# Performance work log

Measured on AMD Instinct MI355X. Metric: run time of the kernel, lower is better.

## Reference

```python
import jax, jax.numpy as jnp
import numpy as np

D_MODEL, D_INNER, D_STATE, HEADDIM, NHEADS, D_CONV, EPS = 2048, 4096, 64, 64, 64, 4, 1e-5
CONV_DIM = D_INNER + 2 * D_STATE  # ngroups=1


def setup_inputs() -> dict:
    key = jax.random.key(0)
    ks = jax.random.split(key, 8)
    return {
        "hidden_states": jax.random.normal(ks[0], (2, 2048, D_MODEL), jnp.float32),
        "rms_weight": jnp.ones((D_MODEL,), jnp.float32),
        "in_proj_w": jax.random.normal(ks[1], (2 * D_INNER + 2 * D_STATE + NHEADS, D_MODEL), jnp.float32) * 0.02,
        "conv_w": jax.random.normal(ks[2], (CONV_DIM, D_CONV), jnp.float32) * 0.2,
        "conv_b": jnp.zeros((CONV_DIM,), jnp.float32),
        "dt_bias": jax.random.normal(ks[3], (NHEADS,), jnp.float32) * 0.5,
        "A_log": jax.random.uniform(ks[4], (NHEADS,), jnp.float32, 0.0, 1.0),
        "D": jnp.ones((NHEADS,), jnp.float32),
        "norm_w": jnp.ones((D_INNER,), jnp.float32),
        "out_proj_w": jax.random.normal(ks[5], (D_MODEL, D_INNER), jnp.float32) * 0.02,
    }


def _rmsnorm(x, w, eps=EPS):
    var = jnp.mean(jnp.square(x), axis=-1, keepdims=True)
    return x * jax.lax.rsqrt(var + eps) * w


def reference(hidden_states, rms_weight, in_proj_w, conv_w, conv_b, dt_bias, A_log, D, norm_w, out_proj_w):
    b, l, _ = hidden_states.shape
    residual = hidden_states
    u = _rmsnorm(hidden_states, rms_weight)
    zxbcdt = jnp.einsum("bld,ed->ble", u, in_proj_w)
    z = zxbcdt[..., :D_INNER]
    xBC = zxbcdt[..., D_INNER:D_INNER + CONV_DIM]
    dt = zxbcdt[..., D_INNER + CONV_DIM:]  # (b, l, h)

    # causal depthwise conv1d over seq
    xBC_t = jnp.transpose(xBC, (0, 2, 1))  # (b, c, l)
    kernel = conv_w[:, None, :]  # (c, 1, k)
    xBC_t = jax.lax.conv_general_dilated(
        xBC_t, kernel, window_strides=(1,), padding=[(D_CONV - 1, 0)],
        feature_group_count=CONV_DIM,
        dimension_numbers=("NCH", "OIH", "NCH"))
    xBC = jax.nn.silu(jnp.transpose(xBC_t, (0, 2, 1)) + conv_b)

    x = xBC[..., :D_INNER].reshape(b, l, NHEADS, HEADDIM)
    B = xBC[..., D_INNER:D_INNER + D_STATE]  # (b, l, n)
    C = xBC[..., D_INNER + D_STATE:]         # (b, l, n)

    dt = jax.nn.softplus(dt + dt_bias)  # (b, l, h)
    A = -jnp.exp(A_log)                 # (h,)
    dA = jnp.exp(dt * A)                # (b, l, h)

    # sequential selective scan over time
    def step(state, inp):
        dA_t, dt_t, x_t, B_t, C_t = inp  # (b,h), (b,h), (b,h,p), (b,n), (b,n)
        state = state * dA_t[:, :, None, None] + jnp.einsum(
            "bh,bhp,bn->bhpn", dt_t, x_t, B_t)
        y_t = jnp.einsum("bhpn,bn->bhp", state, C_t)
        return state, y_t

    xs = (jnp.moveaxis(dA, 1, 0), jnp.moveaxis(dt, 1, 0),
          jnp.moveaxis(x, 1, 0), jnp.moveaxis(B, 1, 0), jnp.moveaxis(C, 1, 0))
    state0 = jnp.zeros((b, NHEADS, HEADDIM, D_STATE), hidden_states.dtype)
    _, ys = jax.lax.scan(step, state0, xs)
    y = jnp.moveaxis(ys, 0, 1)  # (b, l, h, p)
    y = y + D[None, None, :, None] * x
    y = y.reshape(b, l, D_INNER)

    # gated RMSNorm, then output projection
    y = _rmsnorm(y * jax.nn.silu(z), norm_w)
    out = jnp.einsum("ble,de->bld", y, out_proj_w)
    return residual + out
```

## Files before the change

### kernel.cpp

```cpp
#include <hip/hip_runtime.h>
#include <stdint.h>

#define DEV static __device__ __forceinline__

typedef __attribute__((ext_vector_type(8))) __bf16 bf16x8;
typedef __attribute__((ext_vector_type(4))) float f32x4;
typedef __attribute__((ext_vector_type(16))) float f32x16;

DEV float b2f(unsigned short u) {
    union { unsigned int i; float f; } v; v.i = ((unsigned int)u) << 16; return v.f;
}
DEV unsigned short f2b(float f) {
    unsigned int u = __builtin_bit_cast(unsigned int, f);
    unsigned int r = (u + 0x7FFFu + ((u >> 16) & 1u)) >> 16;
    return (unsigned short)r;
}
DEV f32x4 mfma16(bf16x8 a, bf16x8 b, f32x4 c) {
    return __builtin_amdgcn_mfma_f32_16x16x32_bf16(a, b, c, 0, 0, 0);
}
DEV f32x16 mfma32(bf16x8 a, bf16x8 b, f32x16 c) {
    return __builtin_amdgcn_mfma_f32_32x32x16_bf16(a, b, c, 0, 0, 0);
}

DEV void gload16(const void* g, void* l) {
    __builtin_amdgcn_global_load_lds(
        (const __attribute__((address_space(1))) void*)g,
        (__attribute__((address_space(3))) void*)l, 16, 0, 0);
}

__global__ __launch_bounds__(256) void k_cvt(
    const float* __restrict__ src, unsigned short* __restrict__ dst)
{
    long i = ((long)blockIdx.x * 256 + threadIdx.x) * 8;
    float4 a = *(const float4*)(src + i);
    float4 b = *(const float4*)(src + i + 4);
    union { uint4 v; unsigned short s[8]; } o;
    o.s[0] = f2b(a.x); o.s[1] = f2b(a.y); o.s[2] = f2b(a.z); o.s[3] = f2b(a.w);
    o.s[4] = f2b(b.x); o.s[5] = f2b(b.y); o.s[6] = f2b(b.z); o.s[7] = f2b(b.w);
    *(uint4*)(dst + i) = o.v;
}

__global__ __launch_bounds__(256) void k_rmsnorm_in(
    const float* __restrict__ h, const float* __restrict__ w,
    unsigned short* __restrict__ u)
{
    int row = blockIdx.x, t = threadIdx.x;
    const float* hp = h + (long)row * 2048 + t * 8;
    float4 a = *(const float4*)hp;
    float4 b = *(const float4*)(hp + 4);
    float x[8] = {a.x, a.y, a.z, a.w, b.x, b.y, b.z, b.w};
    float ss = 0.f;
#pragma unroll
    for (int i = 0; i < 8; i++) ss += x[i] * x[i];
#pragma unroll
    for (int o = 32; o > 0; o >>= 1) ss += __shfl_down(ss, o);
    __shared__ float red[4];
    if ((t & 63) == 0) red[t >> 6] = ss;
    __syncthreads();
    float tot = red[0] + red[1] + red[2] + red[3];
    float scale = rsqrtf(tot * (1.0f / 2048.0f) + 1e-5f);
    float4 wa = *(const float4*)(w + t * 8);
    float4 wb = *(const float4*)(w + t * 8 + 4);
    float wv[8] = {wa.x, wa.y, wa.z, wa.w, wb.x, wb.y, wb.z, wb.w};
    union { uint4 v; unsigned short s[8]; } ow;
#pragma unroll
    for (int i = 0; i < 8; i++) ow.s[i] = f2b(x[i] * scale * wv[i]);
    *(uint4*)(u + (long)row * 2048 + t * 8) = ow.v;
}

__global__ __launch_bounds__(512, 2) void k_gemm256(
    const unsigned short* __restrict__ A, const unsigned short* __restrict__ Bm,
    int K, unsigned short* __restrict__ Cb, int ldc)
{
    __shared__ __align__(16) char lds[131072];
    int tid = threadIdx.x;
    int w = tid >> 6, l = tid & 63;
    int NT = K >> 6, NI = K >> 7;
    long Kb = (long)K * 2;

    int nwg = gridDim.x * gridDim.y;
    int cpx = nwg >> 3;
    int fl = blockIdx.y * gridDim.x + blockIdx.x;
    int swz = (fl & 7) * cpx + (fl >> 3);
    long m0 = (long)(swz % gridDim.x) * 256;
    long n0 = (long)(swz / gridDim.x) * 256;

    int rl = tid >> 3;
    int csw16 = (((tid & 7) ^ (rl & 7)) << 4);
    const char* pA0 = (const char*)A + (m0 + rl) * Kb + csw16;
    const char* pA1 = (const char*)A + (m0 + 64 + rl) * Kb + csw16;
    const char* pB0 = (const char*)Bm + (n0 + rl) * Kb + csw16;
    const char* pB1 = (const char*)Bm + (n0 + 64 + rl) * Kb + csw16;
    int ldst = tid * 16;

#define STG(P0, P1, RGN, kt, half) do { if ((kt) < NT) {                      \
    char* Lr_ = lds + (((kt) & 1) << 16) + (RGN) + ((half) << 14);            \
    long go_ = (long)(half) * 128 * Kb + (long)(kt) * 128;                    \
    gload16((P0) + go_, Lr_ + ldst);                                          \
    gload16((P1) + go_, Lr_ + 8192 + ldst); } } while (0)

    int lq = l >> 4, lr15 = l & 15, key = l & 7;
    int off0 = ((lq ^ key) << 4);
    int off1 = (((4 + lq) ^ key) << 4);
    int aB = ((w >> 2) * 128 + lr15) * 128;
    int bB = 32768 + (((w & 3) * 64 + lr15) * 128);

    bf16x8 aF[4][2], b0F[2][2], b1F[2][2];
    f32x4 acc[8][4];
#pragma unroll
    for (int s = 0; s < 8; s++)
#pragma unroll
        for (int t = 0; t < 4; t++) acc[s][t] = (f32x4){0.f, 0.f, 0.f, 0.f};

#define DS_A(mh, BUF) do {                                                    \
    const char* ba_ = lds + (BUF) + aB + (mh) * 8192;                         \
    _Pragma("unroll") for (int s_ = 0; s_ < 4; s_++) {                        \
        aF[s_][0] = *(const bf16x8*)(ba_ + s_ * 2048 + off0);                 \
        aF[s_][1] = *(const bf16x8*)(ba_ + s_ * 2048 + off1); } } while (0)

#define DS_B(DST, nh, BUF) do {                                               \
    const char* bb_ = lds + (BUF) + bB + (nh) * 4096;                         \
    _Pragma("unroll") for (int t_ = 0; t_ < 2; t_++) {                        \
        DST[t_][0] = *(const bf16x8*)(bb_ + t_ * 2048 + off0);                \
        DST[t_][1] = *(const bf16x8*)(bb_ + t_ * 2048 + off1); } } while (0)

#define MQ(mh, nh, BF) do {                                                   \
    __builtin_amdgcn_s_setprio(1);                                            \
    _Pragma("unroll") for (int kk_ = 0; kk_ < 2; kk_++)                       \
    _Pragma("unroll") for (int s_ = 0; s_ < 4; s_++)                          \
    _Pragma("unroll") for (int t_ = 0; t_ < 2; t_++)                          \
        acc[(mh) * 4 + s_][(nh) * 2 + t_] =                                   \
            mfma16(aF[s_][kk_], BF[t_][kk_], acc[(mh) * 4 + s_][(nh) * 2 + t_]); \
    __builtin_amdgcn_s_setprio(0); } while (0)

#define BAR asm volatile("s_barrier" ::: "memory")
#define LGD asm volatile("s_waitcnt lgkmcnt(0)" ::: "memory")

    STG(pA0, pA1, 0,     0, 0);
    STG(pA0, pA1, 0,     0, 1);
    STG(pB0, pB1, 32768, 0, 0);
    STG(pB0, pB1, 32768, 0, 1);
    STG(pB0, pB1, 32768, 1, 0);
    STG(pB0, pB1, 32768, 1, 1);
    STG(pA0, pA1, 0,     1, 0);
    asm volatile("s_waitcnt vmcnt(6)" ::: "memory");
    BAR;

    for (int it = 0; it < NI; ++it) {
        int k1 = 2 * it + 1, k2 = 2 * it + 2, k3 = 2 * it + 3;
        DS_A(0, 0); DS_B(b0F, 0, 0);
        STG(pA0, pA1, 0, k1, 1);
        BAR; MQ(0, 0, b0F); LGD; BAR;
        DS_B(b1F, 1, 0);
        BAR; MQ(0, 1, b1F); LGD; BAR;
        DS_A(1, 0);
        STG(pB0, pB1, 32768, k2, 0);
        BAR; MQ(1, 1, b1F); LGD; BAR;
        STG(pB0, pB1, 32768, k2, 1);
        BAR; MQ(1, 0, b0F);
        if (it == NI - 1) { asm volatile("s_waitcnt vmcnt(0)" ::: "memory"); }
        else              { asm volatile("s_waitcnt vmcnt(4)" ::: "memory"); }
        BAR;
        DS_A(0, 65536); DS_B(b0F, 0, 65536);
        STG(pA0, pA1, 0, k2, 0);
        BAR; MQ(0, 0, b0F); LGD; BAR;
        DS_B(b1F, 1, 65536);
        STG(pA0, pA1, 0, k2, 1);
        BAR; MQ(0, 1, b1F); LGD; BAR;
        DS_A(1, 65536);
        STG(pB0, pB1, 32768, k3, 0);
        BAR; MQ(1, 1, b1F); LGD; BAR;
        STG(pB0, pB1, 32768, k3, 1);
        STG(pA0, pA1, 0, k3, 0);
        BAR; MQ(1, 0, b0F);
        if (it < NI - 1) { asm volatile("s_waitcnt vmcnt(6)" ::: "memory"); }
        BAR;
    }

    int colb = (w & 3) * 64 + lr15;
    int rowb = (w >> 2) * 128 + lq * 4;
#pragma unroll
    for (int s = 0; s < 8; s++)
#pragma unroll
        for (int t = 0; t < 4; t++) {
            long col = n0 + colb + t * 16;
            long row = m0 + rowb + s * 16;
#pragma unroll
            for (int r = 0; r < 4; r++)
                Cb[(row + r) * ldc + col] = f2b(acc[s][t][r]);
        }
#undef STG
#undef DS_A
#undef DS_B
#undef MQ
#undef BAR
#undef LGD
}

template <int EPI>
__global__ __launch_bounds__(256) void k_gemm_bt(
    const unsigned short* __restrict__ A, const unsigned short* __restrict__ Bm,
    int K, int nvalid, unsigned short* __restrict__ Cb, float* __restrict__ Cf,
    int ldc, const float* __restrict__ Res)
{
    __shared__ __align__(16) unsigned short sA[128 * 64];
    __shared__ __align__(16) unsigned short sB[128 * 64];
    int t = threadIdx.x;
    int w = t >> 6, L = t & 63;

    int flat = blockIdx.y * gridDim.x + blockIdx.x;
    int per = gridDim.x * 8;
    int strip = flat / per;
    int rem = flat - strip * per;
    long m0 = (long)(strip * 8 + (rem & 7)) * 128;
    long n0 = (long)(rem >> 3) * 128;

    int rloc = t >> 3;
    int c16  = t & 7;
    int csw  = c16 ^ (rloc & 7);
    const unsigned short* gAp[4];
    const unsigned short* gBp[4];
#pragma unroll
    for (int i = 0; i < 4; i++) {
        gAp[i] = A + (m0 + i * 32 + rloc) * (long)K + csw * 8;
        long rb = n0 + i * 32 + rloc;
        if (rb >= nvalid) rb = nvalid - 1;
        gBp[i] = Bm + rb * (long)K + csw * 8;
    }
    unsigned short* lA = sA + t * 8;
    unsigned short* lB = sB + t * 8;

    int mw = (w >> 1) * 64, nw = (w & 1) * 64;
    int rowA = mw + (L & 31), rowB = nw + (L & 31);
    int swA = (rowA & 7) << 4, swB = (rowB & 7) << 4;
    int q16 = (L >> 5) * 16;
    const char* pA = (const char*)sA + rowA * 128;
    const char* pB = (const char*)sB + rowB * 128;

    f32x16 acc[2][2];
#pragma unroll
    for (int ti = 0; ti < 2; ti++)
#pragma unroll
        for (int tj = 0; tj < 2; tj++)
#pragma unroll
            for (int r = 0; r < 16; r++) acc[ti][tj][r] = 0.f;

    for (int kt = 0; kt < K; kt += 64) {
#pragma unroll
        for (int i = 0; i < 4; i++) {
            gload16(gAp[i], lA + i * 2048);
            gload16(gBp[i], lB + i * 2048);
            gAp[i] += 64; gBp[i] += 64;
        }
        __syncthreads();
#pragma unroll
        for (int kk = 0; kk < 4; kk++) {
            bf16x8 af[2], bf[2];
#pragma unroll
            for (int ti = 0; ti < 2; ti++)
                af[ti] = *(const bf16x8*)(pA + ti * 4096 + ((q16 + kk * 32) ^ swA));
#pragma unroll
            for (int tj = 0; tj < 2; tj++)
                bf[tj] = *(const bf16x8*)(pB + tj * 4096 + ((q16 + kk * 32) ^ swB));
#pragma unroll
            for (int ti = 0; ti < 2; ti++)
#pragma unroll
                for (int tj = 0; tj < 2; tj++)
                    acc[ti][tj] = mfma32(af[ti], bf[tj], acc[ti][tj]);
        }
        __syncthreads();
    }
    int colL = L & 31;
    int rL = (L >> 5) * 4;
#pragma unroll
    for (int ti = 0; ti < 2; ti++)
#pragma unroll
        for (int tj = 0; tj < 2; tj++) {
            long c = n0 + nw + tj * 32 + colL;
            if (c >= nvalid) continue;
#pragma unroll
            for (int r = 0; r < 16; r++) {
                long row = m0 + mw + ti * 32 + (r & 3) + 8 * (r >> 2) + rL;
                float v = acc[ti][tj][r];
                if (EPI == 0) Cb[row * ldc + c] = f2b(v);
                else          Cf[row * ldc + c] = v + Res[row * ldc + c];
            }
        }
}

__global__ __launch_bounds__(128) void k_conv(
    const unsigned short* __restrict__ zx, const float* __restrict__ cw,
    const float* __restrict__ cb, unsigned short* __restrict__ xbc)
{
    int c = blockIdx.x * 128 + threadIdx.x;
    int b = blockIdx.z;
    int l0 = blockIdx.y * 64;
    float w0 = cw[c * 4 + 0], w1 = cw[c * 4 + 1];
    float w2 = cw[c * 4 + 2], w3 = cw[c * 4 + 3];
    float bias = cb[c];
    const unsigned short* src = zx + ((long)b * 2048) * 8384 + 4096 + c;
    float xm3 = (l0 >= 3) ? b2f(src[(long)(l0 - 3) * 8384]) : 0.f;
    float xm2 = (l0 >= 2) ? b2f(src[(long)(l0 - 2) * 8384]) : 0.f;
    float xm1 = (l0 >= 1) ? b2f(src[(long)(l0 - 1) * 8384]) : 0.f;
    const unsigned short* s2 = src + (long)l0 * 8384;
    unsigned short* dst = xbc + ((long)(b * 2048 + l0)) * 4224 + c;
#pragma unroll 8
    for (int i = 0; i < 64; i++) {
        float xl = b2f(*s2); s2 += 8384;
        float a = xm3 * w0 + xm2 * w1 + xm1 * w2 + xl * w3 + bias;
        a = a / (1.f + expf(-a));
        *dst = f2b(a); dst += 4224;
        xm3 = xm2; xm2 = xm1; xm1 = xl;
    }
}

__global__ __launch_bounds__(256) void k_chunk_state_mfma(
    const unsigned short* __restrict__ xbc, const unsigned short* __restrict__ zxdt,
    const float* __restrict__ dt_bias, const float* __restrict__ A_log,
    unsigned short* __restrict__ Sbuf, float* __restrict__ dAtot)
{
    int blk = blockIdx.x;
    int c = blk & 7, bh = blk >> 3;
    int b = bh >> 6, h = bh & 63;
    int tid = threadIdx.x;
    int w = tid >> 6, L = tid & 63;
    int quad = L >> 4, col = L & 15;
    int rowBlk = (w >> 1) * 32, colBlk = (w & 1) * 32;
    __shared__ __align__(16) unsigned short sXp[64 * 72];
    __shared__ __align__(16) unsigned short sBn[64 * 72];
    __shared__ float sdt[64], sL[64];
    float Ah = expf(A_log[h]);
    float dtb = dt_bias[h];
    f32x4 acc[2][2];
#pragma unroll
    for (int ti = 0; ti < 2; ti++)
#pragma unroll
        for (int tj = 0; tj < 2; tj++) acc[ti][tj] = (f32x4){0.f, 0.f, 0.f, 0.f};
    float sumL = 0.f;

    for (int sub = 0; sub < 4; sub++) {
        int l0 = c * 256 + sub * 64;
        {
            int t = tid >> 2, pc = tid & 3;
            const unsigned short* gX = xbc + (long)(b * 2048 + l0 + t) * 4224 + h * 64 + pc * 16;
            union { uint4 v; unsigned short s[8]; } x0, x1;
            x0.v = *(const uint4*)gX; x1.v = *(const uint4*)(gX + 8);
#pragma unroll
            for (int j = 0; j < 8; j++) {
                sXp[(pc * 16 + j) * 72 + t] = x0.s[j];
                sXp[(pc * 16 + 8 + j) * 72 + t] = x1.s[j];
            }
        }
        if (tid < 64) {
            float raw = b2f(zxdt[((long)(b * 2048 + l0 + tid)) * 8384 + 8320 + h]) + dtb;
            float dtv = (raw > 20.f) ? raw : log1pf(expf(raw));
            float cum = dtv;
#pragma unroll
            for (int off = 1; off < 64; off <<= 1) {
                float v = __shfl_up(cum, off);
                if (tid >= off) cum += v;
            }
            sdt[tid] = dtv;
            sL[tid] = -Ah * cum;
        }
        __syncthreads();
        float Lend = sL[63];
        {
            int t = tid >> 2, nc = tid & 3;
            float wt = sdt[t] * __expf(Lend - sL[t]);
            const unsigned short* gB = xbc + (long)(b * 2048 + l0 + t) * 4224 + 4096 + nc * 16;
            union { uint4 v; unsigned short s[8]; } x0, x1;
            x0.v = *(const uint4*)gB; x1.v = *(const uint4*)(gB + 8);
#pragma unroll
            for (int j = 0; j < 8; j++) {
                sBn[(nc * 16 + j) * 72 + t] = f2b(b2f(x0.s[j]) * wt);
                sBn[(nc * 16 + 8 + j) * 72 + t] = f2b(b2f(x1.s[j]) * wt);
            }
        }
        __syncthreads();
        float e_end = __expf(Lend);
        sumL += Lend;
#pragma unroll
        for (int ti = 0; ti < 2; ti++)
#pragma unroll
            for (int tj = 0; tj < 2; tj++)
#pragma unroll
                for (int r = 0; r < 4; r++) acc[ti][tj][r] *= e_end;
#pragma unroll
        for (int kb = 0; kb < 2; kb++) {
            bf16x8 ax[2], bx[2];
#pragma unroll
            for (int ti = 0; ti < 2; ti++)
                ax[ti] = *(const bf16x8*)(sXp + (rowBlk + ti * 16 + col) * 72 + kb * 32 + quad * 8);
#pragma unroll
            for (int tj = 0; tj < 2; tj++)
                bx[tj] = *(const bf16x8*)(sBn + (colBlk + tj * 16 + col) * 72 + kb * 32 + quad * 8);
#pragma unroll
            for (int ti = 0; ti < 2; ti++)
#pragma unroll
                for (int tj = 0; tj < 2; tj++)
                    acc[ti][tj] = mfma16(ax[ti], bx[tj], acc[ti][tj]);
        }
        __syncthreads();
    }
#pragma unroll
    for (int ti = 0; ti < 2; ti++)
#pragma unroll
        for (int tj = 0; tj < 2; tj++)
#pragma unroll
            for (int r = 0; r < 4; r++) {
                int p = rowBlk + ti * 16 + quad * 4 + r;
                int n = colBlk + tj * 16 + col;
                Sbuf[(long)blk * 4096 + p * 64 + n] = f2b(acc[ti][tj][r]);
            }
    if (tid == 0) dAtot[blk] = __expf(sumL);
}

__global__ __launch_bounds__(256) void k_scan_chunk_mfma(
    const unsigned short* __restrict__ xbc, const unsigned short* __restrict__ zxdt,
    const float* __restrict__ dt_bias, const float* __restrict__ A_log,
    const float* __restrict__ Dv,
    const unsigned short* __restrict__ Sbuf, const float* __restrict__ dAtot,
    unsigned short* __restrict__ yout)
{
    int blk = blockIdx.x;
    int c = blk & 7, bh = blk >> 3;
    int b = bh >> 6, h = bh & 63;
    int tid = threadIdx.x;
    int w = tid >> 6, L = tid & 63;
    int quad = L >> 4, col = L & 15;
    int rowBlk = (w >> 1) * 32, colBlk = (w & 1) * 32;
    __shared__ __align__(16) unsigned short sCm[64 * 72];
    __shared__ __align__(16) unsigned short sBtMs[64 * 72];
    __shared__ __align__(16) unsigned short sXp[64 * 72];
    __shared__ __align__(16) unsigned short sBn[64 * 72];
    __shared__ __align__(16) unsigned short sHb[64 * 72];
    __shared__ float sdt[64], sL[64], sEs[64];
    float Ah = expf(A_log[h]);
    float dtb = dt_bias[h];
    float Dh = Dv[h];

    f32x4 acc_h[2][2];
#pragma unroll
    for (int ti = 0; ti < 2; ti++)
#pragma unroll
        for (int tj = 0; tj < 2; tj++) acc_h[ti][tj] = (f32x4){0.f, 0.f, 0.f, 0.f};
    int sb = bh * 8;
    for (int j = 0; j < c; j++) {
        float d = dAtot[sb + j];
        const unsigned short* Sp = Sbuf + (long)(sb + j) * 4096;
#pragma unroll
        for (int ti = 0; ti < 2; ti++)
#pragma unroll
            for (int tj = 0; tj < 2; tj++)
#pragma unroll
                for (int r = 0; r < 4; r++) {
                    int p = rowBlk + ti * 16 + quad * 4 + r;
                    int n = colBlk + tj * 16 + col;
                    acc_h[ti][tj][r] = acc_h[ti][tj][r] * d + b2f(Sp[p * 64 + n]);
                }
    }

    for (int sub = 0; sub < 4; sub++) {
        int l0 = c * 256 + sub * 64;
        {
            int row = tid >> 2, c4 = tid & 3;
            const unsigned short* gR = xbc + (long)(b * 2048 + l0 + row) * 4224;
            uint4 v0 = *(const uint4*)(gR + 4160 + c4 * 8);
            uint4 v1 = *(const uint4*)(gR + 4160 + (c4 + 4) * 8);
            *(uint4*)(sCm + row * 72 + c4 * 8) = v0;
            *(uint4*)(sCm + row * 72 + (c4 + 4) * 8) = v1;
            uint4 w0 = *(const uint4*)(gR + 4096 + c4 * 8);
            uint4 w1 = *(const uint4*)(gR + 4096 + (c4 + 4) * 8);
            *(uint4*)(sBtMs + row * 72 + c4 * 8) = w0;
            *(uint4*)(sBtMs + row * 72 + (c4 + 4) * 8) = w1;
        }
        {
            int t = tid >> 2, pc = tid & 3;
            const unsigned short* gX = xbc + (long)(b * 2048 + l0 + t) * 4224 + h * 64 + pc * 16;
            union { uint4 v; unsigned short s[8]; } x0, x1;
            x0.v = *(const uint4*)gX; x1.v = *(const uint4*)(gX + 8);
#pragma unroll
            for (int j = 0; j < 8; j++) {
                sXp[(pc * 16 + j) * 72 + t] = x0.s[j];
                sXp[(pc * 16 + 8 + j) * 72 + t] = x1.s[j];
            }
        }
        if (tid < 64) {
            float raw = b2f(zxdt[((long)(b * 2048 + l0 + tid)) * 8384 + 8320 + h]) + dtb;
            float dtv = (raw > 20.f) ? raw : log1pf(expf(raw));
            float cum = dtv;
#pragma unroll
            for (int off = 1; off < 64; off <<= 1) {
                float v = __shfl_up(cum, off);
                if (tid >= off) cum += v;
            }
            sdt[tid] = dtv;
            float l = -Ah * cum;
            sL[tid] = l;
            sEs[tid] = __expf(l);
        }
        __syncthreads();
        float Lend = sL[63];
        {
            int t = tid >> 2, nc = tid & 3;
            float wt = sdt[t] * __expf(Lend - sL[t]);
            const unsigned short* gB = xbc + (long)(b * 2048 + l0 + t) * 4224 + 4096 + nc * 16;
            union { uint4 v; unsigned short s[8]; } x0, x1;
            x0.v = *(const uint4*)gB; x1.v = *(const uint4*)(gB + 8);
#pragma unroll
            for (int j = 0; j < 8; j++) {
                sBn[(nc * 16 + j) * 72 + t] = f2b(b2f(x0.s[j]) * wt);
                sBn[(nc * 16 + 8 + j) * 72 + t] = f2b(b2f(x1.s[j]) * wt);
            }
        }
#pragma unroll
        for (int ti = 0; ti < 2; ti++)
#pragma unroll
            for (int tj = 0; tj < 2; tj++)
#pragma unroll
                for (int r = 0; r < 4; r++) {
                    int p = rowBlk + ti * 16 + quad * 4 + r;
                    int n = colBlk + tj * 16 + col;
                    sHb[p * 72 + n] = f2b(acc_h[ti][tj][r]);
                }
        __syncthreads();
        f32x4 g[2][2];
#pragma unroll
        for (int ti = 0; ti < 2; ti++)
#pragma unroll
            for (int tj = 0; tj < 2; tj++) g[ti][tj] = (f32x4){0.f, 0.f, 0.f, 0.f};
#pragma unroll
        for (int kb = 0; kb < 2; kb++) {
            bf16x8 ac[2], bc[2];
#pragma unroll
            for (int ti = 0; ti < 2; ti++)
                ac[ti] = *(const bf16x8*)(sCm + (rowBlk + ti * 16 + col) * 72 + kb * 32 + quad * 8);
#pragma unroll
            for (int tj = 0; tj < 2; tj++)
                bc[tj] = *(const bf16x8*)(sBtMs + (colBlk + tj * 16 + col) * 72 + kb * 32 + quad * 8);
#pragma unroll
            for (int ti = 0; ti < 2; ti++)
#pragma unroll
                for (int tj = 0; tj < 2; tj++)
                    g[ti][tj] = mfma16(ac[ti], bc[tj], g[ti][tj]);
        }
        __syncthreads();
#pragma unroll
        for (int tj = 0; tj < 2; tj++) {
            int t_idx = colBlk + tj * 16 + col;
            float lt = sL[t_idx], dtt = sdt[t_idx];
#pragma unroll
            for (int ti = 0; ti < 2; ti++)
#pragma unroll
                for (int r = 0; r < 4; r++) {
                    int s_idx = rowBlk + ti * 16 + quad * 4 + r;
                    float m = (t_idx <= s_idx) ? g[ti][tj][r] * dtt * __expf(sL[s_idx] - lt) : 0.f;
                    sBtMs[s_idx * 72 + t_idx] = f2b(m);
                }
        }
        __syncthreads();
        f32x4 yv[2][2];
#pragma unroll
        for (int ti = 0; ti < 2; ti++)
#pragma unroll
            for (int tj = 0; tj < 2; tj++) yv[ti][tj] = (f32x4){0.f, 0.f, 0.f, 0.f};
#pragma unroll
        for (int kb = 0; kb < 2; kb++) {
            bf16x8 am[2], bxp[2];
#pragma unroll
            for (int ti = 0; ti < 2; ti++)
                am[ti] = *(const bf16x8*)(sBtMs + (rowBlk + ti * 16 + col) * 72 + kb * 32 + quad * 8);
#pragma unroll
            for (int tj = 0; tj < 2; tj++)
                bxp[tj] = *(const bf16x8*)(sXp + (colBlk + tj * 16 + col) * 72 + kb * 32 + quad * 8);
#pragma unroll
            for (int ti = 0; ti < 2; ti++)
#pragma unroll
                for (int tj = 0; tj < 2; tj++)
                    yv[ti][tj] = mfma16(am[ti], bxp[tj], yv[ti][tj]);
        }
        float es0 = sEs[rowBlk + col], es1 = sEs[rowBlk + 16 + col];
#pragma unroll
        for (int kb = 0; kb < 2; kb++) {
            bf16x8 acx[2], bhh[2];
#pragma unroll
            for (int ti = 0; ti < 2; ti++) {
                union { bf16x8 v; unsigned short s[8]; } a;
                a.v = *(const bf16x8*)(sCm + (rowBlk + ti * 16 + col) * 72 + kb * 32 + quad * 8);
                float es = ti ? es1 : es0;
#pragma unroll
                for (int j = 0; j < 8; j++) a.s[j] = f2b(b2f(a.s[j]) * es);
                acx[ti] = a.v;
            }
#pragma unroll
            for (int tj = 0; tj < 2; tj++)
                bhh[tj] = *(const bf16x8*)(sHb + (colBlk + tj * 16 + col) * 72 + kb * 32 + quad * 8);
#pragma unroll
            for (int ti = 0; ti < 2; ti++)
#pragma unroll
                for (int tj = 0; tj < 2; tj++)
                    yv[ti][tj] = mfma16(acx[ti], bhh[tj], yv[ti][tj]);
        }
        float e_end = __expf(Lend);
#pragma unroll
        for (int ti = 0; ti < 2; ti++)
#pragma unroll
            for (int tj = 0; tj < 2; tj++)
#pragma unroll
                for (int r = 0; r < 4; r++) acc_h[ti][tj][r] *= e_end;
#pragma unroll
        for (int kb = 0; kb < 2; kb++) {
            bf16x8 ax[2], bn[2];
#pragma unroll
            for (int ti = 0; ti < 2; ti++)
                ax[ti] = *(const bf16x8*)(sXp + (rowBlk + ti * 16 + col) * 72 + kb * 32 + quad * 8);
#pragma unroll
            for (int tj = 0; tj < 2; tj++)
                bn[tj] = *(const bf16x8*)(sBn + (colBlk + tj * 16 + col) * 72 + kb * 32 + quad * 8);
#pragma unroll
            for (int ti = 0; ti < 2; ti++)
#pragma unroll
                for (int tj = 0; tj < 2; tj++)
                    acc_h[ti][tj] = mfma16(ax[ti], bn[tj], acc_h[ti][tj]);
        }
#pragma unroll
        for (int ti = 0; ti < 2; ti++)
#pragma unroll
            for (int tj = 0; tj < 2; tj++)
#pragma unroll
                for (int r = 0; r < 4; r++) {
                    int s_idx = rowBlk + ti * 16 + quad * 4 + r;
                    int p = colBlk + tj * 16 + col;
                    float xv = b2f(sXp[p * 72 + s_idx]);
                    float yo = yv[ti][tj][r] + Dh * xv;
                    yout[((long)(b * 2048 + l0 + s_idx)) * 8384 + 4096 + h * 64 + p] = f2b(yo);
                }
        __syncthreads();
    }
}

__global__ __launch_bounds__(256) void k_gatenorm(
    const unsigned short* __restrict__ zx, const float* __restrict__ nw,
    unsigned short* __restrict__ y2)
{
    int row = blockIdx.x, t = threadIdx.x;
    const unsigned short* zr = zx + (long)row * 8384;
    float v[16]; float ss = 0.f;
#pragma unroll
    for (int i = 0; i < 16; i++) {
        int c = t + i * 256;
        float z = b2f(zr[c]);
        float y = b2f(zr[4096 + c]);
        float g = y * (z / (1.f + expf(-z)));
        v[i] = g; ss += g * g;
    }
#pragma unroll
    for (int o = 32; o > 0; o >>= 1) ss += __shfl_down(ss, o);
    __shared__ float red[4];
    if ((t & 63) == 0) red[t >> 6] = ss;
    __syncthreads();
    float tot = red[0] + red[1] + red[2] + red[3];
    float scale = rsqrtf(tot * (1.0f / 4096.0f) + 1e-5f);
#pragma unroll
    for (int i = 0; i < 16; i++) {
        int c = t + i * 256;
        y2[(long)row * 4096 + c] = f2b(v[i] * scale * nw[c]);
    }
}

extern "C" void kernel_launch(void* const* d_in, const int* in_sizes, int n_in,
                              void* d_out, int out_size, void* d_ws, size_t ws_size,
                              hipStream_t stream)
{
    const float* h    = (const float*)d_in[0];
    const float* rmsw = (const float*)d_in[1];
    const float* w1   = (const float*)d_in[2];
    const float* cw   = (const float*)d_in[3];
    const float* cbp  = (const float*)d_in[4];
    const float* dtb  = (const float*)d_in[5];
    const float* alog = (const float*)d_in[6];
    const float* Dv   = (const float*)d_in[7];
    const float* nw   = (const float*)d_in[8];
    const float* w2   = (const float*)d_in[9];

    char* ws = (char*)d_ws;
    unsigned short* zx    = (unsigned short*)ws;
    unsigned short* w1b   = (unsigned short*)(ws + 68681728L);
    unsigned short* xbc   = (unsigned short*)(ws + 68681728L);
    unsigned short* y2    = (unsigned short*)(ws + 68681728L);
    unsigned short* u     = (unsigned short*)(ws + 103284736L);
    unsigned short* Sbuf  = (unsigned short*)(ws + 103284736L);
    float*          dAt   = (float*)(ws + 111673344L);
    unsigned short* w2b   = (unsigned short*)(ws + 103284736L);
    float* outp = (float*)d_out;

    k_rmsnorm_in<<<4096, 256, 0, stream>>>(h, rmsw, u);
    k_cvt<<<8384, 256, 0, stream>>>(w1, w1b);
    k_gemm256<<<dim3(16, 32), 512, 0, stream>>>(u, w1b, 2048, zx, 8384);
    k_gemm_bt<0><<<dim3(2, 32), 256, 0, stream>>>(
        u, w1b + 8192L * 2048, 2048, 192, zx + 8192, nullptr, 8384, nullptr);
    k_conv<<<dim3(33, 32, 2), 128, 0, stream>>>(zx, cw, cbp, xbc);
    k_chunk_state_mfma<<<1024, 256, 0, stream>>>(xbc, zx, dtb, alog, Sbuf, dAt);
    k_scan_chunk_mfma<<<1024, 256, 0, stream>>>(xbc, zx, dtb, alog, Dv, Sbuf, dAt, zx);
    k_gatenorm<<<4096, 256, 0, stream>>>(zx, nw, y2);
    k_cvt<<<4096, 256, 0, stream>>>(w2, w2b);
    k_gemm_bt<1><<<dim3(16, 32), 256, 0, stream>>>(y2, w2b, 4096, 2048, nullptr, outp, 2048, h);
}
```

Measured before the change: 523.6 us.

## Drop redundant GEMM barriers, stage epilogue via swizzled LDS, vectorize gatenorm

Removes the barrier placed before each MFMA quarter in the main GEMM loop, keeping only the one after each LDS wait. The GEMM epilogue now writes bf16 results into XOR-swizzled shared memory and then stores full 16-byte rows to global memory, replacing scattered 2-byte stores. The gated-norm kernel switches to 16-byte vector loads and stores with contiguous per-thread chunks. Removing barriers risks LDS read/write races if the double-buffer schedule relied on them, and the epilogue assumes the tile fits in the LDS buffer.

```diff
diff --git a/kernel.cpp b/kernel.cpp
--- a/kernel.cpp
+++ b/kernel.cpp
@@ -150,45 +150,62 @@
         int k1 = 2 * it + 1, k2 = 2 * it + 2, k3 = 2 * it + 3;
         DS_A(0, 0); DS_B(b0F, 0, 0);
         STG(pA0, pA1, 0, k1, 1);
-        BAR; MQ(0, 0, b0F); LGD; BAR;
+        MQ(0, 0, b0F); LGD; BAR;
         DS_B(b1F, 1, 0);
-        BAR; MQ(0, 1, b1F); LGD; BAR;
+        MQ(0, 1, b1F); LGD; BAR;
         DS_A(1, 0);
         STG(pB0, pB1, 32768, k2, 0);
-        BAR; MQ(1, 1, b1F); LGD; BAR;
+        MQ(1, 1, b1F); LGD; BAR;
         STG(pB0, pB1, 32768, k2, 1);
-        BAR; MQ(1, 0, b0F);
+        MQ(1, 0, b0F);
         if (it == NI - 1) { asm volatile("s_waitcnt vmcnt(0)" ::: "memory"); }
         else              { asm volatile("s_waitcnt vmcnt(4)" ::: "memory"); }
         BAR;
         DS_A(0, 65536); DS_B(b0F, 0, 65536);
         STG(pA0, pA1, 0, k2, 0);
-        BAR; MQ(0, 0, b0F); LGD; BAR;
+        MQ(0, 0, b0F); LGD; BAR;
         DS_B(b1F, 1, 65536);
         STG(pA0, pA1, 0, k2, 1);
-        BAR; MQ(0, 1, b1F); LGD; BAR;
+        MQ(0, 1, b1F); LGD; BAR;
         DS_A(1, 65536);
         STG(pB0, pB1, 32768, k3, 0);
-        BAR; MQ(1, 1, b1F); LGD; BAR;
+        MQ(1, 1, b1F); LGD; BAR;
         STG(pB0, pB1, 32768, k3, 1);
         STG(pA0, pA1, 0, k3, 0);
-        BAR; MQ(1, 0, b0F);
+        MQ(1, 0, b0F);
         if (it < NI - 1) { asm volatile("s_waitcnt vmcnt(6)" ::: "memory"); }
         BAR;
     }
 
-    int colb = (w & 3) * 64 + lr15;
-    int rowb = (w >> 2) * 128 + lq * 4;
-#pragma unroll
-    for (int s = 0; s < 8; s++)
-#pragma unroll
-        for (int t = 0; t < 4; t++) {
-            long col = n0 + colb + t * 16;
-            long row = m0 + rowb + s * 16;
-#pragma unroll
-            for (int r = 0; r < 4; r++)
-                Cb[(row + r) * ldc + col] = f2b(acc[s][t][r]);
-        }
+    {
+        unsigned short* sc = (unsigned short*)lds;
+        int rb = (w >> 2) * 128 + lq * 4;
+        int cb2 = (w & 3) * 64 + lr15;
+#pragma unroll
+        for (int s = 0; s < 8; s++)
+#pragma unroll
+            for (int t = 0; t < 4; t++) {
+                int col = cb2 + t * 16;
+#pragma unroll
+                for (int r = 0; r < 4; r++) {
+                    int row = rb + s * 16 + r;
+                    int k9 = (row ^ (row >> 3)) & 7;
+                    int slot = (col >> 3) ^ k9;
+                    sc[row * 256 + slot * 8 + (col & 7)] = f2b(acc[s][t][r]);
+                }
+            }
+        LGD; BAR;
+        int rr = tid >> 1, hh = tid & 1;
+        int k9r = (rr ^ (rr >> 3)) & 7;
+        long base = (m0 + rr) * (long)ldc + n0;
+#pragma unroll
+        for (int i = 0; i < 16; i++) {
+            int slot = hh * 16 + i;
+            int ps = slot ^ k9r;
+            uint4 v = *(const uint4*)(sc + rr * 256 + ps * 8);
+            *(uint4*)(Cb + base + slot * 8) = v;
+        }
+    }
 #undef STG
 #undef DS_A
 #undef DS_B
@@ -646,14 +663,23 @@
 {
     int row = blockIdx.x, t = threadIdx.x;
     const unsigned short* zr = zx + (long)row * 8384;
+    union { uint4 v; unsigned short s[8]; } za, zb, ya, yb;
+    za.v = *(const uint4*)(zr + t * 16);
+    zb.v = *(const uint4*)(zr + t * 16 + 8);
+    ya.v = *(const uint4*)(zr + 4096 + t * 16);
+    yb.v = *(const uint4*)(zr + 4096 + t * 16 + 8);
     float v[16]; float ss = 0.f;
 #pragma unroll
-    for (int i = 0; i < 16; i++) {
-        int c = t + i * 256;
-        float z = b2f(zr[c]);
-        float y = b2f(zr[4096 + c]);
-        float g = y * (z / (1.f + expf(-z)));
+    for (int i = 0; i < 8; i++) {
+        float z = b2f(za.s[i]);
+        float g = b2f(ya.s[i]) * (z / (1.f + expf(-z)));
         v[i] = g; ss += g * g;
+    }
+#pragma unroll
+    for (int i = 0; i < 8; i++) {
+        float z = b2f(zb.s[i]);
+        float g = b2f(yb.s[i]) * (z / (1.f + expf(-z)));
+        v[8 + i] = g; ss += g * g;
     }
 #pragma unroll
     for (int o = 32; o > 0; o >>= 1) ss += __shfl_down(ss, o);
@@ -662,11 +688,20 @@
     __syncthreads();
     float tot = red[0] + red[1] + red[2] + red[3];
     float scale = rsqrtf(tot * (1.0f / 4096.0f) + 1e-5f);
-#pragma unroll
-    for (int i = 0; i < 16; i++) {
-        int c = t + i * 256;
-        y2[(long)row * 4096 + c] = f2b(v[i] * scale * nw[c]);
-    }
+    float4 n0 = *(const float4*)(nw + t * 16);
+    float4 n1 = *(const float4*)(nw + t * 16 + 4);
+    float4 n2 = *(const float4*)(nw + t * 16 + 8);
+    float4 n3 = *(const float4*)(nw + t * 16 + 12);
+    float nv[16] = {n0.x, n0.y, n0.z, n0.w, n1.x, n1.y, n1.z, n1.w,
+                    n2.x, n2.y, n2.z, n2.w, n3.x, n3.y, n3.z, n3.w};
+    union { uint4 u4; unsigned short s[8]; } o0, o1;
+#pragma unroll
+    for (int i = 0; i < 8; i++) o0.s[i] = f2b(v[i] * scale * nv[i]);
+#pragma unroll
+    for (int i = 0; i < 8; i++) o1.s[i] = f2b(v[8 + i] * scale * nv[8 + i]);
+    unsigned short* yo = y2 + (long)row * 4096 + t * 16;
+    *(uint4*)yo = o0.u4;
+    *(uint4*)(yo + 8) = o1.u4;
 }
 
 extern "C" void kernel_launch(void* const* d_in, const int* in_sizes, int n_in,
```

New measurement: 528.5 us. Within noise of the previous version (+0.9%).
